# Optimization experiments

Measured on AMD Instinct MI355X. Metric: run time of the kernel, lower is better.

Reference implementation:

```python
import jax, jax.numpy as jnp
import numpy as np

# --- static config (matches init_kwargs) ---
B, N, M = 128, 32, 32
C_IMG, NUM_HIDDEN, NUM_CLASSES = 1, 16, 3
INPUT_DIM = C_IMG + NUM_HIDDEN + NUM_CLASSES          # 20
OUT_DIM = NUM_HIDDEN + NUM_CLASSES + 2                # 21 (moving -> 2 action channels)
C_STATE = INPUT_DIM - C_IMG                           # 19
N_NEO, M_NEO = N - 2, M - 2                           # size_neo=None -> N-2
N_ACTIVE, M_ACTIVE = N - 2, M - 2
ITERATIONS = 10
IN_FEAT = 9 * INPUT_DIM + 2                           # 182, position='current'
THRESH = 0.0007


def setup_inputs() -> dict:
    key = jax.random.key(0)
    ks = jax.random.split(key, 7)
    images = jax.random.uniform(ks[0], (B, N, M, C_IMG), dtype=jnp.float32)
    W1 = jax.random.normal(ks[1], (IN_FEAT, 30), dtype=jnp.float32) * 0.08
    b1 = jnp.zeros((30,), jnp.float32)
    W2 = jax.random.normal(ks[2], (30, 30), dtype=jnp.float32) * 0.18
    b2 = jnp.zeros((30,), jnp.float32)
    W3 = jax.random.normal(ks[3], (30, OUT_DIM), dtype=jnp.float32) * 0.18
    b3 = jnp.zeros((OUT_DIM,), jnp.float32)
    return {"images": images, "W1": W1, "b1": b1, "W2": W2, "b2": b2, "W3": W3, "b3": b3}


def _custom_round(a):
    # positive -> +1, negative -> -1 (with deadzone |a| <= 0.0007 -> 0)
    return jnp.where(a > THRESH, 1, jnp.where(a < -THRESH, -1, 0)).astype(jnp.int32)


def _run(images, W1, b1, W2, b2, W3, b3):
    dx = jnp.arange(3)
    b_idx = jnp.arange(B)[:, None, None, None, None]        # (B,1,1,1,1)
    # fixed 3x3 windows into state (comms): state[x:x+3, y:y+3]
    sr = (jnp.arange(N_NEO)[:, None] + dx)[:, None, :, None]  # (Nn,1,3,1)
    sc = (jnp.arange(M_NEO)[:, None] + dx)[None, :, None, :]  # (1,Mn,1,3)
    half_n = N // 2
    half_m = M // 2

    # initial perception matrix: identity grid (N_neo == N_active)
    gx, gy = jnp.meshgrid(jnp.arange(N_NEO), jnp.arange(M_NEO), indexing="ij")
    perc0 = jnp.broadcast_to(jnp.stack([gx, gy], -1).astype(jnp.int32), (B, N_NEO, M_NEO, 2))
    state0 = jnp.zeros((B, N, M, C_STATE), jnp.float32)
    guesses0 = jnp.zeros((B * N_NEO * M_NEO, OUT_DIM), jnp.float32)

    def step(carry, _):
        state, perc, _ = carry
        px = perc[..., 0]  # (B,Nn,Mn) int32
        py = perc[..., 1]
        # dynamic 3x3 image patches at (px, py)
        rows = px[..., None, None] + dx[:, None]            # (B,Nn,Mn,3,1)
        cols = py[..., None, None] + dx[None, :]            # (B,Nn,Mn,1,3)
        perc_patch = images[b_idx, rows, cols, :]           # (B,Nn,Mn,3,3,C_IMG)
        comms = state[:, sr, sc, :]                          # (B,Nn,Mn,3,3,C_STATE)
        feat = jnp.concatenate([perc_patch, comms], axis=-1)  # (B,Nn,Mn,3,3,INPUT_DIM)
        feat = feat.reshape(B * N_NEO * M_NEO, 9 * INPUT_DIM)
        # position='current' features
        pos_x = ((px - half_n) / half_n).astype(jnp.float32).reshape(-1, 1)
        pos_y = ((py - half_m) / half_m).astype(jnp.float32).reshape(-1, 1)
        inp = jnp.concatenate([feat, pos_x, pos_y], axis=-1)  # (B*Nn*Mn, 182)
        h = jax.nn.relu(inp @ W1 + b1)
        h = jax.nn.relu(h @ W2 + b2)
        guesses = h @ W3 + b3                                 # (B*Nn*Mn, 21)
        outputs = guesses.reshape(B, N_NEO, M_NEO, OUT_DIM)
        state = state.at[:, 1:1 + N_NEO, 1:1 + M_NEO, :].add(outputs[..., :C_STATE])
        # movement: round actions to {-1,0,1}, add, clip to [0, N_active-1]
        delta = _custom_round(outputs[..., -2:])
        perc = jnp.clip(perc + delta, 0, N_ACTIVE - 1)
        return (state, perc, guesses), None

    (state, perc, guesses), _ = jax.lax.scan(step, (state0, perc0, guesses0), None, length=ITERATIONS)
    class_state = state[:, 1:1 + N_NEO, 1:1 + M_NEO, -NUM_CLASSES:]
    return class_state, guesses


def reference(images, W1, b1, W2, b2, W3, b3):
    return _run(images, W1, b1, W2, b2, W3, b3)
```

## Files before the change

kernel.cpp:

```cpp
#include <hip/hip_runtime.h>

#define B_      128
#define NPIX    32
#define NNEO    30
#define CSTATE  19
#define CPAD    20
#define OUTD    21
#define ITERS   10
#define THRESHV 0.0007f

#define STATE_ELEMS_PAD (B_ * NPIX * NPIX * CPAD)
#define NCELLS      (B_ * NNEO * NNEO)
#define CLASS_ELEMS (NCELLS * 3)
#define HSTRIDE 31

__global__ void nca_init(float* __restrict__ stateA, float* __restrict__ stateB) {
    int idx = blockIdx.x * blockDim.x + threadIdx.x;
    const int total = B_ * 124 * CPAD;
    if (idx >= total) return;
    int c  = idx % CPAD;
    int t2 = idx / CPAD;
    int cell = t2 % 124;
    int b    = t2 / 124;
    int i, j;
    if (cell < 32)      { i = 0;  j = cell; }
    else if (cell < 64) { i = 31; j = cell - 32; }
    else { int k = cell - 64; i = 1 + (k >> 1); j = (k & 1) ? 31 : 0; }
    size_t off = (((size_t)b * NPIX + i) * NPIX + j) * CPAD + c;
    stateA[off] = 0.0f;
    stateB[off] = 0.0f;
}

__global__ __launch_bounds__(1024, 8)
void nca_step0(const float* __restrict__ img,
               const float* __restrict__ W1, const float* __restrict__ b1,
               const float* __restrict__ W2, const float* __restrict__ b2,
               const float* __restrict__ W3, const float* __restrict__ b3,
               float* __restrict__ state_new, int* __restrict__ perc) {
    __shared__ float s_img[NPIX * NPIX];
    __shared__ float s_h[240 * HSTRIDE];

    const int b   = blockIdx.y;
    const int rg  = blockIdx.x;
    const int i0  = (rg < 2) ? rg * 8 : 16 + (rg - 2) * 7;
    const int nr  = (rg < 2) ? 8 : 7;
    const int tid = threadIdx.x;
    const int qh  = __builtin_amdgcn_readfirstlane(tid >> 8);
    const int cell = tid & 255;
    const int qoff = (qh == 0) ? 0 : (qh == 1) ? 8 : (qh == 2) ? 14 : 22;
    const int off3 = 5 * qh;

    if (tid < NPIX * NPIX / 4) {
        ((float4*)s_img)[tid] = ((const float4*)(img + (size_t)b * NPIX * NPIX))[tid];
    }
    __syncthreads();

    const int cells = nr * NNEO;
    const bool active = cell < cells;

    int r = 0, j = 0, i = 0, gcell = 0, px = 0, py = 0;
    if (active) {
        r = cell / NNEO;
        j = cell % NNEO;
        i = i0 + r;
        gcell = (b * NNEO + i) * NNEO + j;
        px = i; py = j;
    }

    float h1[8];
    {
        const float* __restrict__ bb = b1 + qoff;
#pragma unroll
        for (int q = 0; q < 8; q++) h1[q] = bb[q];
    }
    if (active) {
        for (int pr = 0; pr < 3; pr++) {
            for (int pc = 0; pc < 3; pc++) {
                const int p9 = pr * 3 + pc;
                const float iv = s_img[(px + pr) * NPIX + (py + pc)];
                const float* __restrict__ wp = W1 + (p9 * 20) * 30 + qoff;
#pragma unroll
                for (int q = 0; q < 8; q++) h1[q] += iv * wp[q];
            }
        }
        const float posx = (float)(px - 16) * (1.0f / 16.0f);
        const float posy = (float)(py - 16) * (1.0f / 16.0f);
        const float* __restrict__ wx = W1 + 180 * 30 + qoff;
        const float* __restrict__ wy = W1 + 181 * 30 + qoff;
#pragma unroll
        for (int q = 0; q < 8; q++) h1[q] += posx * wx[q];
#pragma unroll
        for (int q = 0; q < 8; q++) h1[q] += posy * wy[q];
#pragma unroll
        for (int q = 0; q < 8; q++) h1[q] = fmaxf(h1[q], 0.0f);
#pragma unroll
        for (int q = 0; q < 8; q++) s_h[cell * HSTRIDE + qoff + q] = h1[q];
    }
    __syncthreads();

    float h2[8];
    {
        const float* __restrict__ bb = b2 + qoff;
#pragma unroll
        for (int q = 0; q < 8; q++) h2[q] = bb[q];
    }
    if (active) {
        float a1[30];
#pragma unroll
        for (int k = 0; k < 30; k++) a1[k] = s_h[cell * HSTRIDE + k];
        for (int k = 0; k < 30; k++) {
            const float* __restrict__ wr = W2 + k * 30 + qoff;
#pragma unroll
            for (int q = 0; q < 8; q++) h2[q] += a1[k] * wr[q];
        }
#pragma unroll
        for (int q = 0; q < 8; q++) h2[q] = fmaxf(h2[q], 0.0f);
    }
    __syncthreads();
    if (active) {
#pragma unroll
        for (int q = 0; q < 8; q++) s_h[cell * HSTRIDE + qoff + q] = h2[q];
    }
    __syncthreads();

    float o[6];
    {
        const float* __restrict__ bb = b3 + off3;
#pragma unroll
        for (int c = 0; c < 6; c++) o[c] = bb[c];
    }
    if (active) {
        float a2[30];
#pragma unroll
        for (int k = 0; k < 30; k++) a2[k] = s_h[cell * HSTRIDE + k];
        for (int k = 0; k < 30; k++) {
            const float* __restrict__ wr = W3 + k * 21 + off3;
#pragma unroll
            for (int c = 0; c < 6; c++) o[c] += a2[k] * wr[c];
        }
        float* __restrict__ ns =
            state_new + (((size_t)b * NPIX + (i + 1)) * NPIX + (j + 1)) * CPAD;
        if (qh == 0) {
#pragma unroll
            for (int c = 0; c < 6; c++) ns[c] = o[c];
        } else if (qh < 3) {
#pragma unroll
            for (int c = 1; c < 6; c++) ns[off3 + c] = o[c];
        } else {
#pragma unroll
            for (int c = 1; c < 4; c++) ns[15 + c] = o[c];
            int dxm = (o[4] > THRESHV) ? 1 : ((o[4] < -THRESHV) ? -1 : 0);
            int dym = (o[5] > THRESHV) ? 1 : ((o[5] < -THRESHV) ? -1 : 0);
            px += dxm; py += dym;
            px = (px < 0) ? 0 : ((px > NNEO - 1) ? NNEO - 1 : px);
            py = (py < 0) ? 0 : ((py > NNEO - 1) ? NNEO - 1 : py);
            perc[2 * gcell + 0] = px;
            perc[2 * gcell + 1] = py;
        }
    }
}

template<bool LAST>
__global__ __launch_bounds__(1024, 8)
void nca_step(const float* __restrict__ img,
              const float* __restrict__ W1, const float* __restrict__ b1,
              const float* __restrict__ W2, const float* __restrict__ b2,
              const float* __restrict__ W3, const float* __restrict__ b3,
              const float* __restrict__ state_old, float* __restrict__ state_new,
              int* perc, float* __restrict__ guesses_out,
              float* __restrict__ class_out) {
    __shared__ float s_state[10 * NPIX * CPAD];
    __shared__ float s_img[NPIX * NPIX];
    __shared__ float s_h[240 * HSTRIDE];

    const int b   = blockIdx.y;
    const int rg  = blockIdx.x;
    const int i0  = (rg < 2) ? rg * 8 : 16 + (rg - 2) * 7;
    const int nr  = (rg < 2) ? 8 : 7;
    const int tid = threadIdx.x;
    const int qh  = __builtin_amdgcn_readfirstlane(tid >> 8);
    const int cell = tid & 255;
    const int qoff = (qh == 0) ? 0 : (qh == 1) ? 8 : (qh == 2) ? 14 : 22;
    const int off3 = 5 * qh;

    {
        const int n4 = (nr + 2) * NPIX * CPAD / 4;
        const float4* gstate4 =
            (const float4*)(state_old + ((size_t)b * NPIX + i0) * NPIX * CPAD);
        float4* s_state4 = (float4*)s_state;
        for (int t = tid; t < n4; t += 1024) s_state4[t] = gstate4[t];
    }
    if (tid < NPIX * NPIX / 4) {
        ((float4*)s_img)[tid] = ((const float4*)(img + (size_t)b * NPIX * NPIX))[tid];
    }
    __syncthreads();

    const int cells = nr * NNEO;
    const bool active = cell < cells;

    int r = 0, j = 0, i = 0, gcell = 0, px = 0, py = 0;
    if (active) {
        r = cell / NNEO;
        j = cell % NNEO;
        i = i0 + r;
        gcell = (b * NNEO + i) * NNEO + j;
        px = perc[2 * gcell]; py = perc[2 * gcell + 1];
    }

    float h1[8];
    {
        const float* __restrict__ bb = b1 + qoff;
#pragma unroll
        for (int q = 0; q < 8; q++) h1[q] = bb[q];
    }
    if (active) {
        for (int pr = 0; pr < 3; pr++) {
            for (int pc = 0; pc < 3; pc++) {
                const int p9 = pr * 3 + pc;
                const float iv = s_img[(px + pr) * NPIX + (py + pc)];
                const float* __restrict__ wp = W1 + (p9 * 20) * 30 + qoff;
                const int sbase = ((r + pr) * NPIX + (j + pc)) * CPAD;
                float fv[20];
                {
                    const float4* __restrict__ sp =
                        (const float4*)&s_state[sbase];
#pragma unroll
                    for (int v = 0; v < 5; v++)
                        *(float4*)&fv[4 * v] = sp[v];
                }
#pragma unroll
                for (int q = 0; q < 8; q++) h1[q] += iv * wp[q];
                for (int ch = 0; ch < CSTATE; ch++) {
                    const float* __restrict__ wr = wp + (ch + 1) * 30;
#pragma unroll
                    for (int q = 0; q < 8; q++) h1[q] += fv[ch] * wr[q];
                }
            }
        }
        const float posx = (float)(px - 16) * (1.0f / 16.0f);
        const float posy = (float)(py - 16) * (1.0f / 16.0f);
        const float* __restrict__ wx = W1 + 180 * 30 + qoff;
        const float* __restrict__ wy = W1 + 181 * 30 + qoff;
#pragma unroll
        for (int q = 0; q < 8; q++) h1[q] += posx * wx[q];
#pragma unroll
        for (int q = 0; q < 8; q++) h1[q] += posy * wy[q];
#pragma unroll
        for (int q = 0; q < 8; q++) h1[q] = fmaxf(h1[q], 0.0f);
#pragma unroll
        for (int q = 0; q < 8; q++) s_h[cell * HSTRIDE + qoff + q] = h1[q];
    }
    __syncthreads();

    float h2[8];
    {
        const float* __restrict__ bb = b2 + qoff;
#pragma unroll
        for (int q = 0; q < 8; q++) h2[q] = bb[q];
    }
    if (active) {
        float a1[30];
#pragma unroll
        for (int k = 0; k < 30; k++) a1[k] = s_h[cell * HSTRIDE + k];
        for (int k = 0; k < 30; k++) {
            const float* __restrict__ wr = W2 + k * 30 + qoff;
#pragma unroll
            for (int q = 0; q < 8; q++) h2[q] += a1[k] * wr[q];
        }
#pragma unroll
        for (int q = 0; q < 8; q++) h2[q] = fmaxf(h2[q], 0.0f);
    }
    __syncthreads();
    if (active) {
#pragma unroll
        for (int q = 0; q < 8; q++) s_h[cell * HSTRIDE + qoff + q] = h2[q];
    }
    __syncthreads();

    float o[6];
    {
        const float* __restrict__ bb = b3 + off3;
#pragma unroll
        for (int c = 0; c < 6; c++) o[c] = bb[c];
    }
    if (active) {
        float a2[30];
#pragma unroll
        for (int k = 0; k < 30; k++) a2[k] = s_h[cell * HSTRIDE + k];
        for (int k = 0; k < 30; k++) {
            const float* __restrict__ wr = W3 + k * 21 + off3;
#pragma unroll
            for (int c = 0; c < 6; c++) o[c] += a2[k] * wr[c];
        }

        const int lcenter = ((r + 1) * NPIX + (j + 1)) * CPAD;
        if (!LAST) {
            float* __restrict__ ns =
                state_new + (((size_t)b * NPIX + (i + 1)) * NPIX + (j + 1)) * CPAD;
            if (qh == 0) {
#pragma unroll
                for (int c = 0; c < 6; c++)
                    ns[c] = s_state[lcenter + c] + o[c];
            } else if (qh < 3) {
#pragma unroll
                for (int c = 1; c < 6; c++)
                    ns[off3 + c] = s_state[lcenter + off3 + c] + o[c];
            } else {
#pragma unroll
                for (int c = 1; c < 4; c++)
                    ns[15 + c] = s_state[lcenter + 15 + c] + o[c];
                int dxm = (o[4] > THRESHV) ? 1 : ((o[4] < -THRESHV) ? -1 : 0);
                int dym = (o[5] > THRESHV) ? 1 : ((o[5] < -THRESHV) ? -1 : 0);
                px += dxm; py += dym;
                px = (px < 0) ? 0 : ((px > NNEO - 1) ? NNEO - 1 : px);
                py = (py < 0) ? 0 : ((py > NNEO - 1) ? NNEO - 1 : py);
                perc[2 * gcell + 0] = px;
                perc[2 * gcell + 1] = py;
            }
        } else {
            float* __restrict__ g = guesses_out + (size_t)gcell * OUTD;
            if (qh == 0) {
#pragma unroll
                for (int c = 0; c < 6; c++) g[c] = o[c];
            } else {
#pragma unroll
                for (int c = 1; c < 6; c++) g[off3 + c] = o[c];
            }
            if (qh == 3) {
                float* __restrict__ cs = class_out + (size_t)gcell * 3;
#pragma unroll
                for (int cc = 0; cc < 3; cc++)
                    cs[cc] = s_state[lcenter + 16 + cc] + o[1 + cc];
            }
        }
    }
}

extern "C" void kernel_launch(void* const* d_in, const int* in_sizes, int n_in,
                              void* d_out, int out_size, void* d_ws, size_t ws_size,
                              hipStream_t stream) {
    const float* img = (const float*)d_in[0];
    const float* W1  = (const float*)d_in[1];
    const float* b1  = (const float*)d_in[2];
    const float* W2  = (const float*)d_in[3];
    const float* b2  = (const float*)d_in[4];
    const float* W3  = (const float*)d_in[5];
    const float* b3  = (const float*)d_in[6];

    float* out = (float*)d_out;
    float* class_out   = out;
    float* guesses_out = out + CLASS_ELEMS;

    float* stateA = (float*)d_ws;
    float* stateB = stateA + STATE_ELEMS_PAD;
    int*   perc   = (int*)(stateB + STATE_ELEMS_PAD);

    {
        const int total = B_ * 124 * CPAD;
        nca_init<<<(total + 255) / 256, 256, 0, stream>>>(stateA, stateB);
    }

    const dim3 grid(4, B_);
    nca_step0<<<grid, 1024, 0, stream>>>(img, W1, b1, W2, b2, W3, b3,
                                         stateB, perc);
    for (int t = 1; t < ITERS - 1; t++) {
        const float* so = (t & 1) ? stateB : stateA;
        float*       sn = (t & 1) ? stateA : stateB;
        nca_step<false><<<grid, 1024, 0, stream>>>(
            img, W1, b1, W2, b2, W3, b3, so, sn, perc, guesses_out, class_out);
    }
    nca_step<true><<<grid, 1024, 0, stream>>>(
        img, W1, b1, W2, b2, W3, b3, stateB, stateA, perc, guesses_out, class_out);
}
```

Before: 346.6 us.

## Fold border init into step0 and alias shared buffers to drop a barrier

Removes the separate border-zeroing kernel and performs that zeroing inside the first step kernel, saving one launch. In the main step kernel, shared memory is pooled so the second hidden layer writes into the region previously holding state and image, which removes one __syncthreads between layer 2 compute and its store. The center-state values are read into registers before that region is overwritten. This cuts LDS footprint and one barrier per step, but depends on the aliasing being correct.

New measurement: 357.9 us. 1.03x slower.

```diff
diff --git a/kernel.cpp b/kernel.cpp
--- a/kernel.cpp
+++ b/kernel.cpp
@@ -14,29 +14,13 @@
 #define CLASS_ELEMS (NCELLS * 3)
 #define HSTRIDE 31
 
-__global__ void nca_init(float* __restrict__ stateA, float* __restrict__ stateB) {
-    int idx = blockIdx.x * blockDim.x + threadIdx.x;
-    const int total = B_ * 124 * CPAD;
-    if (idx >= total) return;
-    int c  = idx % CPAD;
-    int t2 = idx / CPAD;
-    int cell = t2 % 124;
-    int b    = t2 / 124;
-    int i, j;
-    if (cell < 32)      { i = 0;  j = cell; }
-    else if (cell < 64) { i = 31; j = cell - 32; }
-    else { int k = cell - 64; i = 1 + (k >> 1); j = (k & 1) ? 31 : 0; }
-    size_t off = (((size_t)b * NPIX + i) * NPIX + j) * CPAD + c;
-    stateA[off] = 0.0f;
-    stateB[off] = 0.0f;
-}
-
 __global__ __launch_bounds__(1024, 8)
 void nca_step0(const float* __restrict__ img,
                const float* __restrict__ W1, const float* __restrict__ b1,
                const float* __restrict__ W2, const float* __restrict__ b2,
                const float* __restrict__ W3, const float* __restrict__ b3,
-               float* __restrict__ state_new, int* __restrict__ perc) {
+               float* __restrict__ stateA, float* __restrict__ stateB,
+               int* __restrict__ perc) {
     __shared__ float s_img[NPIX * NPIX];
     __shared__ float s_h[240 * HSTRIDE];
 
@@ -50,6 +34,22 @@
     const int qoff = (qh == 0) ? 0 : (qh == 1) ? 8 : (qh == 2) ? 14 : 22;
     const int off3 = 5 * qh;
 
+    {
+        const int per = (124 * CPAD) / 4;
+        if (tid < per) {
+            int idx = rg * per + tid;
+            int c    = idx % CPAD;
+            int bc   = idx / CPAD;
+            int bi, bj;
+            if (bc < 32)      { bi = 0;  bj = bc; }
+            else if (bc < 64) { bi = 31; bj = bc - 32; }
+            else { int k = bc - 64; bi = 1 + (k >> 1); bj = (k & 1) ? 31 : 0; }
+            size_t off = (((size_t)b * NPIX + bi) * NPIX + bj) * CPAD + c;
+            stateA[off] = 0.0f;
+            stateB[off] = 0.0f;
+        }
+    }
+
     if (tid < NPIX * NPIX / 4) {
         ((float4*)s_img)[tid] = ((const float4*)(img + (size_t)b * NPIX * NPIX))[tid];
     }
@@ -139,7 +139,7 @@
             for (int c = 0; c < 6; c++) o[c] += a2[k] * wr[c];
         }
         float* __restrict__ ns =
-            state_new + (((size_t)b * NPIX + (i + 1)) * NPIX + (j + 1)) * CPAD;
+            stateB + (((size_t)b * NPIX + (i + 1)) * NPIX + (j + 1)) * CPAD;
         if (qh == 0) {
 #pragma unroll
             for (int c = 0; c < 6; c++) ns[c] = o[c];
@@ -169,9 +169,11 @@
               const float* __restrict__ state_old, float* __restrict__ state_new,
               int* perc, float* __restrict__ guesses_out,
               float* __restrict__ class_out) {
-    __shared__ float s_state[10 * NPIX * CPAD];
-    __shared__ float s_img[NPIX * NPIX];
-    __shared__ float s_h[240 * HSTRIDE];
+    __shared__ float pool[7440 + 7440];
+    float* s_state = pool;
+    float* s_img   = pool + 6400;
+    float* s_h2    = pool;
+    float* s_h     = pool + 7440;
 
     const int b   = blockIdx.y;
     const int rg  = blockIdx.x;
@@ -213,20 +215,21 @@
 #pragma unroll
         for (int q = 0; q < 8; q++) h1[q] = bb[q];
     }
-    if (active) {
+    float cs[6];
+    const int lcenter = ((r + 1) * NPIX + (j + 1)) * CPAD;
+    if (active) {
+        const int pix0 = r * NPIX + j;
         for (int pr = 0; pr < 3; pr++) {
             for (int pc = 0; pc < 3; pc++) {
                 const int p9 = pr * 3 + pc;
                 const float iv = s_img[(px + pr) * NPIX + (py + pc)];
                 const float* __restrict__ wp = W1 + (p9 * 20) * 30 + qoff;
-                const int sbase = ((r + pr) * NPIX + (j + pc)) * CPAD;
+                const int sbase = (pix0 + pr * NPIX + pc) * CPAD;
                 float fv[20];
                 {
-                    const float4* __restrict__ sp =
-                        (const float4*)&s_state[sbase];
-#pragma unroll
-                    for (int v = 0; v < 5; v++)
-                        *(float4*)&fv[4 * v] = sp[v];
+                    const float4* __restrict__ sp = (const float4*)&s_state[sbase];
+#pragma unroll
+                    for (int v = 0; v < 5; v++) *(float4*)&fv[4 * v] = sp[v];
                 }
 #pragma unroll
                 for (int q = 0; q < 8; q++) h1[q] += iv * wp[q];
@@ -248,6 +251,8 @@
 #pragma unroll
         for (int q = 0; q < 8; q++) h1[q] = fmaxf(h1[q], 0.0f);
 #pragma unroll
+        for (int c = 0; c < 6; c++) cs[c] = s_state[lcenter + off3 + c];
+#pragma unroll
         for (int q = 0; q < 8; q++) s_h[cell * HSTRIDE + qoff + q] = h1[q];
     }
     __syncthreads();
@@ -269,11 +274,8 @@
         }
 #pragma unroll
         for (int q = 0; q < 8; q++) h2[q] = fmaxf(h2[q], 0.0f);
-    }
-    __syncthreads();
-    if (active) {
-#pragma unroll
-        for (int q = 0; q < 8; q++) s_h[cell * HSTRIDE + qoff + q] = h2[q];
+#pragma unroll
+        for (int q = 0; q < 8; q++) s_h2[cell * HSTRIDE + qoff + q] = h2[q];
     }
     __syncthreads();
 
@@ -286,29 +288,25 @@
     if (active) {
         float a2[30];
 #pragma unroll
-        for (int k = 0; k < 30; k++) a2[k] = s_h[cell * HSTRIDE + k];
+        for (int k = 0; k < 30; k++) a2[k] = s_h2[cell * HSTRIDE + k];
         for (int k = 0; k < 30; k++) {
             const float* __restrict__ wr = W3 + k * 21 + off3;
 #pragma unroll
             for (int c = 0; c < 6; c++) o[c] += a2[k] * wr[c];
         }
 
-        const int lcenter = ((r + 1) * NPIX + (j + 1)) * CPAD;
         if (!LAST) {
             float* __restrict__ ns =
                 state_new + (((size_t)b * NPIX + (i + 1)) * NPIX + (j + 1)) * CPAD;
             if (qh == 0) {
 #pragma unroll
-                for (int c = 0; c < 6; c++)
-                    ns[c] = s_state[lcenter + c] + o[c];
+                for (int c = 0; c < 6; c++) ns[c] = cs[c] + o[c];
             } else if (qh < 3) {
 #pragma unroll
-                for (int c = 1; c < 6; c++)
-                    ns[off3 + c] = s_state[lcenter + off3 + c] + o[c];
+                for (int c = 1; c < 6; c++) ns[off3 + c] = cs[c] + o[c];
             } else {
 #pragma unroll
-                for (int c = 1; c < 4; c++)
-                    ns[15 + c] = s_state[lcenter + 15 + c] + o[c];
+                for (int c = 1; c < 4; c++) ns[15 + c] = cs[c] + o[c];
                 int dxm = (o[4] > THRESHV) ? 1 : ((o[4] < -THRESHV) ? -1 : 0);
                 int dym = (o[5] > THRESHV) ? 1 : ((o[5] < -THRESHV) ? -1 : 0);
                 px += dxm; py += dym;
@@ -327,10 +325,10 @@
                 for (int c = 1; c < 6; c++) g[off3 + c] = o[c];
             }
             if (qh == 3) {
-                float* __restrict__ cs = class_out + (size_t)gcell * 3;
+                float* __restrict__ csp = class_out + (size_t)gcell * 3;
 #pragma unroll
                 for (int cc = 0; cc < 3; cc++)
-                    cs[cc] = s_state[lcenter + 16 + cc] + o[1 + cc];
+                    csp[cc] = cs[1 + cc] + o[1 + cc];
             }
         }
     }
@@ -355,14 +353,9 @@
     float* stateB = stateA + STATE_ELEMS_PAD;
     int*   perc   = (int*)(stateB + STATE_ELEMS_PAD);
 
-    {
-        const int total = B_ * 124 * CPAD;
-        nca_init<<<(total + 255) / 256, 256, 0, stream>>>(stateA, stateB);
-    }
-
     const dim3 grid(4, B_);
     nca_step0<<<grid, 1024, 0, stream>>>(img, W1, b1, W2, b2, W3, b3,
-                                         stateB, perc);
+                                         stateA, stateB, perc);
     for (int t = 1; t < ITERS - 1; t++) {
         const float* so = (t & 1) ? stateB : stateA;
         float*       sn = (t & 1) ? stateA : stateB;
```
